# Kernel tuning notes

Hardware: AMD Instinct MI355X
Metric: run time of the kernel (lower is better)

## Reference

```python
import jax, jax.numpy as jnp
import numpy as np
from functools import partial

SEQ, BS, IN, H, A = 1024, 512, 128, 256, 3
NEG_INF = jnp.float32(-1e8)


def setup_inputs() -> dict:
    key = jax.random.key(0)
    ks = jax.random.split(key, 16)
    g = lambda k, shape, s=0.1: (jax.random.normal(k, shape, dtype=jnp.float32) * s)
    inp = {
        "x": jax.random.normal(ks[0], (SEQ * BS, IN), dtype=jnp.float32),
        "done": jax.random.randint(ks[1], (SEQ * BS,), 0, 2, dtype=jnp.int32),
        "invalid_action_mask": jax.random.randint(ks[2], (SEQ * BS, A), 0, 2).astype(bool),
        "h0": jnp.zeros((1, BS, H), jnp.float32),
        "c0": jnp.zeros((1, BS, H), jnp.float32),
        # LSTM params (torch gate order: i, f, g, o)
        "W_ih": g(ks[3], (4 * H, IN)),
        "W_hh": g(ks[4], (4 * H, H)),
        "b_ih": jnp.zeros((4 * H,), jnp.float32),
        "b_hh": jnp.zeros((4 * H,), jnp.float32),
        # action head MLP: H -> H/2 -> H/2 -> A with tanh
        "Wa1": g(ks[5], (H // 2, H)), "ba1": jnp.zeros((H // 2,), jnp.float32),
        "Wa2": g(ks[6], (H // 2, H // 2)), "ba2": jnp.zeros((H // 2,), jnp.float32),
        "Wa3": g(ks[7], (A, H // 2)), "ba3": jnp.zeros((A,), jnp.float32),
        # value head MLP: H -> H/2 -> H/2 -> 1 with tanh
        "Wv1": g(ks[8], (H // 2, H)), "bv1": jnp.zeros((H // 2,), jnp.float32),
        "Wv2": g(ks[9], (H // 2, H // 2)), "bv2": jnp.zeros((H // 2,), jnp.float32),
        "Wv3": g(ks[10], (1, H // 2)), "bv3": jnp.zeros((1,), jnp.float32),
    }
    return inp


def _mlp(h, W1, b1, W2, b2, W3, b3):
    h = jnp.tanh(h @ W1.T + b1)
    h = jnp.tanh(h @ W2.T + b2)
    return h @ W3.T + b3


def _scan_lstm(x, done_f, h0, c0, W_ih, W_hh, b_ih, b_hh):
    batch = h0.shape[1]
    xs = x.reshape(-1, batch, x.shape[-1])        # (T, BS, IN) time-major
    ds = done_f.reshape(-1, batch)                # (T, BS)
    b = b_ih + b_hh

    def step(carry, inp):
        h, c = carry
        xt, dt = inp
        m = (1.0 - dt)[:, None]                   # reset mask before step
        h = h * m
        c = c * m
        gates = xt @ W_ih.T + h @ W_hh.T + b      # (BS, 4H)
        i, f, gg, o = jnp.split(gates, 4, axis=-1)
        c = jax.nn.sigmoid(f) * c + jax.nn.sigmoid(i) * jnp.tanh(gg)
        h = jax.nn.sigmoid(o) * jnp.tanh(c)
        return (h, c), h

    (hn, cn), hs = jax.lax.scan(step, (h0[0], c0[0]), (xs, ds))
    hidden = hs.reshape(-1, h0.shape[-1])         # (T*BS, H), time-major like torch cat
    return hidden, hn[None], cn[None]


def reference(x, done, invalid_action_mask, h0, c0, W_ih, W_hh, b_ih, b_hh,
              Wa1, ba1, Wa2, ba2, Wa3, ba3, Wv1, bv1, Wv2, bv2, Wv3, bv3):
    done_f = done.astype(x.dtype)
    hidden, hn, cn = _scan_lstm(x, done_f, h0, c0, W_ih, W_hh, b_ih, b_hh)
    logits = _mlp(hidden, Wa1, ba1, Wa2, ba2, Wa3, ba3)
    # CategoricalMasked: masks = ~invalid_action_mask, masked logits -> -1e8
    logits = jnp.where(~invalid_action_mask, logits, NEG_INF)
    value = _mlp(hidden, Wv1, bv1, Wv2, bv2, Wv3, bv3)
    return logits, value, hn, cn
```

## Files before the change

### kernel.cpp

```cpp
#include <hip/hip_runtime.h>
#include <hip/hip_bf16.h>
#include <stdint.h>
#include <stddef.h>


typedef short bf16x8 __attribute__((ext_vector_type(8)));
typedef short bf16x4 __attribute__((ext_vector_type(4)));
typedef float f32x4  __attribute__((ext_vector_type(4)));

#define LOG2E 1.44269504088896340736f

__device__ __forceinline__ float fexp2(float x){ return __builtin_amdgcn_exp2f(x); }
__device__ __forceinline__ float frcpf_(float x){ return __builtin_amdgcn_rcpf(x); }
__device__ __forceinline__ float fsig(float x){ return frcpf_(1.0f + fexp2(-x*LOG2E)); }
__device__ __forceinline__ float ftanh_(float x){ return 1.0f - 2.0f*frcpf_(1.0f + fexp2(x*(2.0f*LOG2E))); }

__device__ __forceinline__ short f2bf(float f){
  unsigned u = __builtin_bit_cast(unsigned, f);
  u += 0x7fffu + ((u>>16)&1u);
  return (short)(u>>16);
}
__device__ __forceinline__ float bf2f(short h){
  unsigned u = ((unsigned)(unsigned short)h)<<16;
  return __builtin_bit_cast(float, u);
}

static constexpr size_t WS_WMAIN  = 0;
static constexpr size_t WS_WA1P   = 786432;
static constexpr size_t WS_WV1P   = 851968;
static constexpr size_t WS_WA2P   = 917504;
static constexpr size_t WS_WV2P   = 950272;
static constexpr size_t WS_BMAIN  = 983040;
static constexpr size_t WS_META   = 1048576;
static constexpr size_t WS_SEGS   = 1081344;
static constexpr size_t WS_SORTED = 3178496;
static constexpr size_t WS_HID    = 5275648;
static constexpr size_t WS_NEED_SPLIT = WS_HID + 268435456;

__global__ void k0a_packmain(const float* __restrict__ wih, const float* __restrict__ whh,
                             const float* __restrict__ bih, const float* __restrict__ bhh,
                             short* __restrict__ wp, float* __restrict__ bp)
{
  int tidg = blockIdx.x*512 + threadIdx.x;
  {
    int lane = tidg & 63;
    int nt   = (tidg>>6) & 15;
    int ci   = tidg>>10;
    int kt = ci>>2, gq = ci&3;
    int gs = lane & 15;
    int ug = gs>>2, eg = gs&3;
    int j  = gq*64 + ug*16 + nt;
    int g  = eg*256 + j;
    int k0 = kt*32 + (lane>>4)*8;
    bf16x8 ov;
#pragma unroll
    for (int jj=0;jj<8;++jj){
      int k = k0 + jj;
      float v = (k < 128) ? wih[(size_t)g*128 + k] : whh[(size_t)g*256 + (k-128)];
      ov[jj] = f2bf(v);
    }
    *(bf16x8*)(wp + (size_t)tidg*8) = ov;
  }
  if (tidg < 1024) {
    int cgp = tidg;
    int gq = cgp>>8, nt = (cgp>>4)&15, ug = (cgp>>2)&3, eg = cgp&3;
    int g = eg*256 + gq*64 + ug*16 + nt;
    bp[cgp] = bih[g] + bhh[g];
  }
}

__global__ void k0b_packheads(const float* __restrict__ wa1, const float* __restrict__ wv1,
                              const float* __restrict__ wa2, const float* __restrict__ wv2,
                              short* __restrict__ wa1p, short* __restrict__ wv1p,
                              short* __restrict__ wa2p, short* __restrict__ wv2p)
{
  int p = blockIdx.x*512 + threadIdx.x;
  const float* src; short* dst; int K; int pl;
  if (p < 4096)       { src=wa1; dst=wa1p; K=256; pl=p; }
  else if (p < 8192)  { src=wv1; dst=wv1p; K=256; pl=p-4096; }
  else if (p < 10240) { src=wa2; dst=wa2p; K=128; pl=p-8192; }
  else                { src=wv2; dst=wv2p; K=128; pl=p-10240; }
  int lane = pl & 63;
  int f    = pl >> 6;
  int nt   = f & 7;
  int kt   = f >> 3;
  int n  = nt*16 + (lane&15);
  int k0 = kt*32 + (lane>>4)*8;
  bf16x8 ov;
#pragma unroll
  for (int j=0;j<8;++j) ov[j] = f2bf(src[(size_t)n*K + k0 + j]);
  *(bf16x8*)(dst + (size_t)pl*8) = ov;
}

__global__ void k1_maskmode(const unsigned char* __restrict__ mask, uint32_t* __restrict__ flag)
{
  int i = blockIdx.x*256 + threadIdx.x;
  uint32_t v = ((i & 3) != 0) ? (uint32_t)mask[i] : 0u;
  if (v) atomicOr((unsigned int*)flag, 1u);
}

__global__ void k2a_segments(const int* __restrict__ done, uint32_t* __restrict__ segs,
                             uint32_t* __restrict__ nSegs)
{
  const int b = blockIdx.x;
  const int tid = threadIdx.x;
  __shared__ uint16_t starts[1025];
  __shared__ uint32_t cnts[256];
  __shared__ uint32_t basePos;

  uint32_t my[4]; int myn = 0;
  int t0 = tid*4;
#pragma unroll
  for (int i=0;i<4;++i){
    int t = t0 + i;
    int d = done[(size_t)t*512 + b];
    if (t == 0 || d != 0) my[myn++] = (uint32_t)t;
  }
  cnts[tid] = (uint32_t)myn;
  __syncthreads();
  for (int off=1; off<256; off<<=1){
    uint32_t v = (tid >= off) ? cnts[tid-off] : 0u;
    __syncthreads();
    cnts[tid] += v;
    __syncthreads();
  }
  uint32_t myBase = cnts[tid] - (uint32_t)myn;
  uint32_t ns = cnts[255];
  for (int i=0;i<myn;++i) starts[myBase+i] = (uint16_t)my[i];
  if (tid == 0) {
    starts[ns] = 1024;
    basePos = atomicAdd((unsigned int*)nSegs, ns);
  }
  __syncthreads();
  for (uint32_t i = tid; i < ns; i += 256) {
    uint32_t st = starts[i];
    uint32_t ln = (uint32_t)starts[i+1] - st;
    segs[basePos + i] = ((ln-1u)<<19) | (st<<9) | (uint32_t)b;
  }
}

__global__ void k2b_hist(const uint32_t* __restrict__ segs, const uint32_t* __restrict__ nSegs,
                         uint32_t* __restrict__ hist)
{
  __shared__ uint32_t lh[1025];
  const uint32_t n = *nSegs;
  for (int i = threadIdx.x; i < 1025; i += 512) lh[i] = 0;
  __syncthreads();
  for (uint32_t i = blockIdx.x*512u + threadIdx.x; i < n; i += gridDim.x*512u) {
    uint32_t ln = ((segs[i]>>19)&1023u) + 1u;
    atomicAdd(&lh[ln], 1u);
  }
  __syncthreads();
  for (int i = threadIdx.x; i < 1025; i += 512)
    if (lh[i]) atomicAdd((unsigned int*)&hist[i], lh[i]);
}

__global__ void k2c_scan(const uint32_t* __restrict__ hist, uint32_t* __restrict__ curs)
{
  __shared__ uint32_t s[1024];
  const int tid = threadIdx.x;
  uint32_t own = hist[tid+1];
  s[tid] = own;
  __syncthreads();
  for (int off=1; off<1024; off<<=1){
    uint32_t v = (tid+off < 1024) ? s[tid+off] : 0u;
    __syncthreads();
    s[tid] += v;
    __syncthreads();
  }
  curs[tid+1] = s[tid] - own;
  if (tid == 0) curs[0] = 0;
}

__global__ void k2d_scatter(const uint32_t* __restrict__ segs, const uint32_t* __restrict__ nSegs,
                            uint32_t* __restrict__ curs, uint32_t* __restrict__ sorted)
{
  __shared__ uint32_t lh[1025];
  __shared__ uint32_t base[1025];
  const uint32_t n = *nSegs;
  const uint32_t chunk = (n + 127u) >> 7;
  const uint32_t lo = blockIdx.x * chunk;
  const uint32_t hi = (lo + chunk < n) ? (lo + chunk) : n;
  for (int i = threadIdx.x; i < 1025; i += 512) lh[i] = 0;
  __syncthreads();
  for (uint32_t i = lo + threadIdx.x; i < hi; i += 512u) {
    uint32_t ln = ((segs[i]>>19)&1023u) + 1u;
    atomicAdd(&lh[ln], 1u);
  }
  __syncthreads();
  for (int i = threadIdx.x; i < 1025; i += 512) {
    uint32_t c = lh[i];
    if (c) base[i] = atomicAdd((unsigned int*)&curs[i], c);
    lh[i] = 0;
  }
  __syncthreads();
  for (uint32_t i = lo + threadIdx.x; i < hi; i += 512u) {
    uint32_t r = segs[i];
    uint32_t ln = ((r>>19)&1023u) + 1u;
    uint32_t pos = base[ln] + atomicAdd(&lh[ln], 1u);
    sorted[pos] = r;
  }
}

__global__ __launch_bounds__(512, 2) void k3r_lstm(
    const float* __restrict__ x, const int* __restrict__ done,
    const float* __restrict__ h0, const float* __restrict__ c0,
    const short* __restrict__ wpack, const float* __restrict__ bpack,
    const uint32_t* __restrict__ sortedSegs, const uint32_t* __restrict__ nSegsPtr,
    short* __restrict__ hidden, float* __restrict__ hnOut, float* __restrict__ cnOut)
{
  __shared__ char smem[54016];
  char* Alds = smem;
  float* biasL = (float*)(smem + 49152);
  uint32_t* meta = (uint32_t*)(smem + 53248);

  const int tid  = threadIdx.x;
  const int lane = tid & 63;
  const int wv   = tid >> 6;
  const int gq   = wv & 3;
  const int rh   = wv >> 2;
  const int cl   = lane & 15;
  const int u    = lane >> 4;
  const int ku   = u*16;
  const int swc  = (cl & 7) << 4;
  const int rA   = rh*32 + cl;
  const int rB   = rA + 16;
  const int jb   = gq*64 + u*16;
  const int jb2  = 2*jb;

  const int row8 = tid >> 3;
  const int oct  = tid & 7;
  const int rsw8 = (row8 & 7) << 4;

  biasL[tid]       = bpack[tid];
  biasL[512 + tid] = bpack[512 + tid];

  const uint32_t nSegs = *nSegsPtr;
  const uint32_t nGroups = (nSegs + 63u) >> 6;

  for (uint32_t g = blockIdx.x; g < nGroups; g += gridDim.x) {
    __syncthreads();
    if (tid < 64) {
      uint32_t idx = g*64u + (uint32_t)tid;
      uint32_t b=0, st=0, ln=0;
      if (idx < nSegs) {
        uint32_t r = sortedSegs[idx];
        b = r & 511u; st = (r>>9)&1023u; ln = ((r>>19)&1023u) + 1u;
      }
      meta[tid] = b; meta[64+tid] = st; meta[128+tid] = ln;
    }
    __syncthreads();

    const uint32_t mb8  = meta[row8];
    const uint32_t mst8 = meta[64+row8];
    const uint32_t mln8 = meta[128+row8];
    const uint32_t mbA  = meta[rA],    mbB  = meta[rB];
    const uint32_t mstA = meta[64+rA], mstB = meta[64+rB];
    const uint32_t mlnA = meta[128+rA],mlnB = meta[128+rB];
    const int maxLen = (int)meta[128];

    {
      const bool act = (mln8 > 0u);
      float xf[16];
      if (act) {
        const float4* xp = (const float4*)(x + ((size_t)mst8*512u + mb8)*128u + (size_t)oct*16u);
#pragma unroll
        for (int i=0;i<4;++i){ float4 t4 = xp[i]; xf[4*i]=t4.x; xf[4*i+1]=t4.y; xf[4*i+2]=t4.z; xf[4*i+3]=t4.w; }
      } else {
#pragma unroll
        for (int i=0;i<16;++i) xf[i]=0.0f;
      }
      bf16x8 v0, v1;
#pragma unroll
      for (int j=0;j<8;++j){ v0[j]=f2bf(xf[j]); v1[j]=f2bf(xf[8+j]); }
      *(bf16x8*)(Alds + row8*768 + ((oct*32     ) ^ rsw8)) = v0;
      *(bf16x8*)(Alds + row8*768 + ((oct*32 + 16) ^ rsw8)) = v1;

      const bool useInit = act && (mst8 == 0u) && (done[mb8] == 0);
      float hf[32];
      if (useInit) {
        const float4* hp = (const float4*)(h0 + (size_t)mb8*256u + (size_t)oct*32u);
#pragma unroll
        for (int i=0;i<8;++i){ float4 t4 = hp[i]; hf[4*i]=t4.x; hf[4*i+1]=t4.y; hf[4*i+2]=t4.z; hf[4*i+3]=t4.w; }
      } else {
#pragma unroll
        for (int i=0;i<32;++i) hf[i]=0.0f;
      }
#pragma unroll
      for (int q=0;q<4;++q){
        bf16x8 hv;
#pragma unroll
        for (int j=0;j<8;++j) hv[j]=f2bf(hf[q*8+j]);
        *(bf16x8*)(Alds + row8*768 + ((256 + oct*64 + q*16) ^ rsw8)) = hv;
      }
    }

    float cregA[16], cregB[16];
    {
      const bool initA = (mlnA > 0u) && (mstA == 0u) && (done[mbA] == 0);
      const bool initB = (mlnB > 0u) && (mstB == 0u) && (done[mbB] == 0);
      f32x4 ca[4], cb[4];
#pragma unroll
      for (int q=0;q<4;++q){
        ca[q] = initA ? *(const f32x4*)(c0 + (size_t)mbA*256u + jb + q*4) : (f32x4){0.f,0.f,0.f,0.f};
        cb[q] = initB ? *(const f32x4*)(c0 + (size_t)mbB*256u + jb + q*4) : (f32x4){0.f,0.f,0.f,0.f};
      }
#pragma unroll
      for (int nt=0;nt<16;++nt){ cregA[nt]=ca[nt>>2][nt&3]; cregB[nt]=cb[nt>>2][nt&3]; }
    }

    for (int it = 0; it < maxLen; ++it) {
      __syncthreads();

      if (it >= 1 && (uint32_t)(it-1) < mln8) {
        const size_t grow = (size_t)(mst8 + (uint32_t)(it-1))*512u + mb8;
        short* hp = hidden + grow*256u + (size_t)oct*32u;
#pragma unroll
        for (int q=0;q<4;++q)
          *(bf16x8*)(hp + q*8) = *(const bf16x8*)(Alds + row8*768 + ((256 + oct*64 + q*16) ^ rsw8));
      }

      f32x4 accA[16], accB[16];
#pragma unroll
      for (int nt=0;nt<16;++nt){
        f32x4 bv = *(const f32x4*)(biasL + gq*256 + nt*16 + u*4);
        accA[nt]=bv; accB[nt]=bv;
      }
      for (int kt=0; kt<12; ++kt) {
        if ((kt & 3) == 0) __builtin_amdgcn_s_barrier();
        const short* wkt = wpack + (size_t)(kt*4 + gq)*8192 + lane*8;
        bf16x8 bfA = *(const bf16x8*)(Alds + rA*768 + ((kt*64 + ku) ^ swc));
        bf16x8 bfB = *(const bf16x8*)(Alds + rB*768 + ((kt*64 + ku) ^ swc));
#pragma unroll
        for (int nt=0;nt<16;++nt) {
          const bf16x8 wf = *(const bf16x8*)(wkt + nt*512);
          accA[nt] = __builtin_amdgcn_mfma_f32_16x16x32_bf16(wf, bfA, accA[nt], 0,0,0);
          accB[nt] = __builtin_amdgcn_mfma_f32_16x16x32_bf16(wf, bfB, accB[nt], 0,0,0);
        }
      }

      bf16x8 xpre0, xpre1;
      {
        const bool xact = (it + 1) < (int)mln8;
        if (xact) {
          const float4* xp = (const float4*)(x + ((size_t)(mst8+it+1u)*512u + mb8)*128u + (size_t)oct*16u);
          float4 a0=xp[0], a1=xp[1], a2=xp[2], a3=xp[3];
          xpre0[0]=f2bf(a0.x); xpre0[1]=f2bf(a0.y); xpre0[2]=f2bf(a0.z); xpre0[3]=f2bf(a0.w);
          xpre0[4]=f2bf(a1.x); xpre0[5]=f2bf(a1.y); xpre0[6]=f2bf(a1.z); xpre0[7]=f2bf(a1.w);
          xpre1[0]=f2bf(a2.x); xpre1[1]=f2bf(a2.y); xpre1[2]=f2bf(a2.z); xpre1[3]=f2bf(a2.w);
          xpre1[4]=f2bf(a3.x); xpre1[5]=f2bf(a3.y); xpre1[6]=f2bf(a3.z); xpre1[7]=f2bf(a3.w);
        } else {
#pragma unroll
          for (int j=0;j<8;++j){ xpre0[j]=0; xpre1[j]=0; }
        }
      }

      __syncthreads();

      const bool finA = (it == (int)mlnA - 1) && (mstA + mlnA == 1024u) && (mlnA > 0u);
      const bool finB = (it == (int)mlnB - 1) && (mstB + mlnB == 1024u) && (mlnB > 0u);
      bf16x8 hvA0, hvA1, hvB0, hvB1;
#pragma unroll
      for (int nt=0;nt<16;++nt) {
        f32x4 gA = accA[nt];
        float i0=fsig(gA[0]), f0=fsig(gA[1]), g0=ftanh_(gA[2]), o0=fsig(gA[3]);
        float cA = f0*cregA[nt] + i0*g0; cregA[nt]=cA;
        float hA = o0*ftanh_(cA);
        if (nt < 8) hvA0[nt] = f2bf(hA); else hvA1[nt-8] = f2bf(hA);
        if (finA) { hnOut[(size_t)mbA*256u + jb + nt] = hA; cnOut[(size_t)mbA*256u + jb + nt] = cA; }
        f32x4 gB = accB[nt];
        float i1=fsig(gB[0]), f1=fsig(gB[1]), g1=ftanh_(gB[2]), o1=fsig(gB[3]);
        float cB = f1*cregB[nt] + i1*g1; cregB[nt]=cB;
        float hB = o1*ftanh_(cB);
        if (nt < 8) hvB0[nt] = f2bf(hB); else hvB1[nt-8] = f2bf(hB);
        if (finB) { hnOut[(size_t)mbB*256u + jb + nt] = hB; cnOut[(size_t)mbB*256u + jb + nt] = cB; }
      }
      *(bf16x8*)(Alds + rA*768 + ((256 + jb2     ) ^ swc)) = hvA0;
      *(bf16x8*)(Alds + rA*768 + ((256 + jb2 + 16) ^ swc)) = hvA1;
      *(bf16x8*)(Alds + rB*768 + ((256 + jb2     ) ^ swc)) = hvB0;
      *(bf16x8*)(Alds + rB*768 + ((256 + jb2 + 16) ^ swc)) = hvB1;

      *(bf16x8*)(Alds + row8*768 + ((oct*32     ) ^ rsw8)) = xpre0;
      *(bf16x8*)(Alds + row8*768 + ((oct*32 + 16) ^ rsw8)) = xpre1;
    }

    __syncthreads();
    if (maxLen > 0 && mln8 == (uint32_t)maxLen) {
      const size_t grow = (size_t)(mst8 + (uint32_t)(maxLen-1))*512u + mb8;
      short* hp = hidden + grow*256u + (size_t)oct*32u;
#pragma unroll
      for (int q=0;q<4;++q)
        *(bf16x8*)(hp + q*8) = *(const bf16x8*)(Alds + row8*768 + ((256 + oct*64 + q*16) ^ rsw8));
    }
  }
}

__global__ __launch_bounds__(512, 1) void k4_heads(
    const short* __restrict__ hidden,
    const short* __restrict__ wa1p, const short* __restrict__ wv1p,
    const short* __restrict__ wa2p, const short* __restrict__ wv2p,
    const float* __restrict__ ba1, const float* __restrict__ bv1,
    const float* __restrict__ ba2, const float* __restrict__ bv2,
    const float* __restrict__ wa3, const float* __restrict__ ba3,
    const float* __restrict__ wv3, const float* __restrict__ bv3,
    const unsigned char* __restrict__ maskB, const uint32_t* __restrict__ maskModePtr,
    float* __restrict__ logits, float* __restrict__ value)
{
  __shared__ char smem[67600];
  char* hidL = smem;
  char* hb1  = smem + 32768;
  char* hb2  = smem + 49152;
  float* w3L = (float*)(smem + 65536);
  float* b3L = (float*)(smem + 67584);

  const int tid  = threadIdx.x;
  const int lane = tid & 63;
  const int wv   = tid >> 6;
  const int gq   = wv & 3;
  const int rh   = wv >> 2;
  const int cl   = lane & 15;
  const int u    = lane >> 4;
  const int ku   = u*16;
  const int swc  = (cl & 7) << 4;
  const int row8 = tid >> 3;
  const int oct  = tid & 7;
  const int rsw8 = (row8 & 7) << 4;
  const size_t r0 = (size_t)blockIdx.x * 64u;

  {
    const short* hp = hidden + (r0 + (size_t)row8)*256u + (size_t)oct*32u;
#pragma unroll
    for (int q=0;q<4;++q)
      *(bf16x8*)(hidL + row8*512 + ((oct*64 + q*16) ^ rsw8)) = *(const bf16x8*)(hp + q*8);
  }
  if (tid < 128) {
    w3L[tid]       = wa3[tid];
    w3L[128 + tid] = wa3[128 + tid];
    w3L[256 + tid] = wa3[256 + tid];
    w3L[384 + tid] = wv3[tid];
  }
  if (tid == 0) { b3L[0]=ba3[0]; b3L[1]=ba3[1]; b3L[2]=ba3[2]; b3L[3]=bv3[0]; }
  const uint32_t maskByteMode = *maskModePtr;
  const int* maskI = (const int*)maskB;
  __syncthreads();

  for (int hd = 0; hd < 2; ++hd) {
    const short* w1p = hd ? wv1p : wa1p;
    const short* w2p = hd ? wv2p : wa2p;
    const float* b1  = hd ? bv1 : ba1;
    const float* b2  = hd ? bv2 : ba2;

    {
      f32x4 h1[2][2];
#pragma unroll
      for (int n1=0;n1<2;++n1){
        f32x4 bv = *(const f32x4*)(b1 + gq*32 + n1*16 + u*4);
        h1[n1][0]=bv; h1[n1][1]=bv;
      }
      for (int kt2=0; kt2<8; ++kt2) {
        bf16x8 bh[2];
#pragma unroll
        for (int r4=0;r4<2;++r4)
          bh[r4] = *(const bf16x8*)(hidL + (rh*32 + r4*16 + cl)*512 + ((kt2*64 + ku) ^ swc));
#pragma unroll
        for (int n1=0;n1<2;++n1) {
          const bf16x8 wf = *(const bf16x8*)(w1p + (size_t)(kt2*8 + gq*2 + n1)*512 + lane*8);
#pragma unroll
          for (int r4=0;r4<2;++r4)
            h1[n1][r4] = __builtin_amdgcn_mfma_f32_16x16x32_bf16(wf, bh[r4], h1[n1][r4], 0,0,0);
        }
      }
#pragma unroll
      for (int n1=0;n1<2;++n1){
#pragma unroll
        for (int r4=0;r4<2;++r4){
          bf16x4 hv;
#pragma unroll
          for (int e=0;e<4;++e) hv[e] = f2bf(ftanh_(h1[n1][r4][e]));
          int row = rh*32 + r4*16 + cl;
          *(bf16x4*)(hb1 + row*256 + ((2*(gq*32 + n1*16 + u*4)) ^ swc)) = hv;
        }
      }
    }
    __syncthreads();

    {
      f32x4 h2[2][2];
#pragma unroll
      for (int n1=0;n1<2;++n1){
        f32x4 bv = *(const f32x4*)(b2 + gq*32 + n1*16 + u*4);
        h2[n1][0]=bv; h2[n1][1]=bv;
      }
      for (int kt2=0; kt2<4; ++kt2) {
        bf16x8 bh[2];
#pragma unroll
        for (int r4=0;r4<2;++r4)
          bh[r4] = *(const bf16x8*)(hb1 + (rh*32 + r4*16 + cl)*256 + ((kt2*64 + ku) ^ swc));
#pragma unroll
        for (int n1=0;n1<2;++n1) {
          const bf16x8 wf = *(const bf16x8*)(w2p + (size_t)(kt2*8 + gq*2 + n1)*512 + lane*8);
#pragma unroll
          for (int r4=0;r4<2;++r4)
            h2[n1][r4] = __builtin_amdgcn_mfma_f32_16x16x32_bf16(wf, bh[r4], h2[n1][r4], 0,0,0);
        }
      }
#pragma unroll
      for (int n1=0;n1<2;++n1){
#pragma unroll
        for (int r4=0;r4<2;++r4){
          bf16x4 hv;
#pragma unroll
          for (int e=0;e<4;++e) hv[e] = f2bf(ftanh_(h2[n1][r4][e]));
          int row = rh*32 + r4*16 + cl;
          *(bf16x4*)(hb2 + row*256 + ((2*(gq*32 + n1*16 + u*4)) ^ swc)) = hv;
        }
      }
    }
    __syncthreads();

    {
      const int row  = tid >> 3;
      const int o    = (tid >> 1) & 3;
      const int half = tid & 1;
      const int sw   = (row&7)<<4;
      float s = half ? 0.0f : b3L[o];
      const float* wr = w3L + o*128 + half*64;
#pragma unroll
      for (int k16=0; k16<8; ++k16) {
        bf16x8 av = *(const bf16x8*)(hb2 + row*256 + (((half*8 + k16)*16) ^ sw));
#pragma unroll
        for (int j=0;j<8;++j) s += bf2f(av[j]) * wr[k16*8+j];
      }
      s += __shfl_xor(s, 1);
      if (half == 0) {
        const size_t grow = r0 + (size_t)row;
        if (hd == 0 && o < 3) {
          const size_t mi = grow*3u + (size_t)o;
          const bool masked = maskByteMode ? (maskB[mi] != 0) : (maskI[mi] != 0);
          logits[mi] = masked ? -1e8f : s;
        } else if (hd == 1 && o == 3) {
          value[grow] = s;
        }
      }
    }
    __syncthreads();
  }
}

__global__ __launch_bounds__(512, 2) void k3_lstm_fused(
    const float* __restrict__ x, const int* __restrict__ done,
    const float* __restrict__ h0, const float* __restrict__ c0,
    const short* __restrict__ wpack, const float* __restrict__ bpack,
    const short* __restrict__ wa1p, const short* __restrict__ wv1p,
    const short* __restrict__ wa2p, const short* __restrict__ wv2p,
    const float* __restrict__ ba1, const float* __restrict__ bv1,
    const float* __restrict__ ba2, const float* __restrict__ bv2,
    const float* __restrict__ wa3, const float* __restrict__ ba3,
    const float* __restrict__ wv3, const float* __restrict__ bv3,
    const unsigned char* __restrict__ maskB,
    const uint32_t* __restrict__ maskModePtr,
    const uint32_t* __restrict__ sortedSegs, const uint32_t* __restrict__ nSegsPtr,
    float* __restrict__ logits, float* __restrict__ value,
    float* __restrict__ hnOut, float* __restrict__ cnOut)
{
  __shared__ char smem[121616];
  char* Alds = smem;
  char* hb1  = smem + 49152;
  char* hb2  = smem + 81920;
  float* biasL = (float*)(smem + 114688);
  uint32_t* meta = (uint32_t*)(smem + 118784);
  float* w3L = (float*)(smem + 119552);
  float* b3L = (float*)(smem + 121600);

  const int tid  = threadIdx.x;
  const int lane = tid & 63;
  const int wv   = tid >> 6;
  const int gq   = wv & 3;
  const int hd   = wv >> 2;
  const int cl   = lane & 15;
  const int u    = lane >> 4;
  const int ku   = u*16;
  const int swc  = (cl & 7) << 4;
  const int rA   = hd*32 + cl;
  const int rB   = rA + 16;
  const int jb   = gq*64 + u*16;
  const int jb2  = 2*jb;

  const int row8 = tid >> 3;
  const int oct  = tid & 7;
  const int rsw8 = (row8 & 7) << 4;

  biasL[tid]       = bpack[tid];
  biasL[512 + tid] = bpack[512 + tid];
  if (tid < 128) {
    w3L[tid]       = wa3[tid];
    w3L[128 + tid] = wa3[128 + tid];
    w3L[256 + tid] = wa3[256 + tid];
    w3L[384 + tid] = wv3[tid];
  }
  if (tid == 0) { b3L[0]=ba3[0]; b3L[1]=ba3[1]; b3L[2]=ba3[2]; b3L[3]=bv3[0]; }

  float4 bH1v[2], bH2v[2];
  {
    const float* b1 = hd ? bv1 : ba1;
    const float* b2 = hd ? bv2 : ba2;
#pragma unroll
    for (int n1=0; n1<2; ++n1) {
      bH1v[n1] = *(const float4*)(b1 + gq*32 + n1*16 + u*4);
      bH2v[n1] = *(const float4*)(b2 + gq*32 + n1*16 + u*4);
    }
  }
  const short* w1p = hd ? wv1p : wa1p;
  const short* w2p = hd ? wv2p : wa2p;

  const uint32_t maskByteMode = *maskModePtr;
  const int* maskI = (const int*)maskB;

  const uint32_t nSegs = *nSegsPtr;
  const uint32_t nGroups = (nSegs + 63u) >> 6;

  for (uint32_t g = blockIdx.x; g < nGroups; g += gridDim.x) {
    __syncthreads();
    if (tid < 64) {
      uint32_t idx = g*64u + (uint32_t)tid;
      uint32_t b=0, st=0, ln=0;
      if (idx < nSegs) {
        uint32_t r = sortedSegs[idx];
        b = r & 511u; st = (r>>9)&1023u; ln = ((r>>19)&1023u) + 1u;
      }
      meta[tid] = b; meta[64+tid] = st; meta[128+tid] = ln;
    }
    __syncthreads();

    const uint32_t mb8  = meta[row8];
    const uint32_t mst8 = meta[64+row8];
    const uint32_t mln8 = meta[128+row8];
    const uint32_t mbA  = meta[rA],    mbB  = meta[rB];
    const uint32_t mstA = meta[64+rA], mstB = meta[64+rB];
    const uint32_t mlnA = meta[128+rA],mlnB = meta[128+rB];
    const int maxLen = (int)meta[128];

    {
      const bool act = (mln8 > 0u);
      float xf[16];
      if (act) {
        const float4* xp = (const float4*)(x + ((size_t)mst8*512u + mb8)*128u + (size_t)oct*16u);
#pragma unroll
        for (int i=0;i<4;++i){ float4 t4 = xp[i]; xf[4*i]=t4.x; xf[4*i+1]=t4.y; xf[4*i+2]=t4.z; xf[4*i+3]=t4.w; }
      } else {
#pragma unroll
        for (int i=0;i<16;++i) xf[i]=0.0f;
      }
      bf16x8 v0, v1;
#pragma unroll
      for (int j=0;j<8;++j){ v0[j]=f2bf(xf[j]); v1[j]=f2bf(xf[8+j]); }
      *(bf16x8*)(Alds + row8*768 + ((oct*32     ) ^ rsw8)) = v0;
      *(bf16x8*)(Alds + row8*768 + ((oct*32 + 16) ^ rsw8)) = v1;

      const bool useInit = act && (mst8 == 0u) && (done[mb8] == 0);
      float hf[32];
      if (useInit) {
        const float4* hp = (const float4*)(h0 + (size_t)mb8*256u + (size_t)oct*32u);
#pragma unroll
        for (int i=0;i<8;++i){ float4 t4 = hp[i]; hf[4*i]=t4.x; hf[4*i+1]=t4.y; hf[4*i+2]=t4.z; hf[4*i+3]=t4.w; }
      } else {
#pragma unroll
        for (int i=0;i<32;++i) hf[i]=0.0f;
      }
#pragma unroll
      for (int q=0;q<4;++q){
        bf16x8 hv;
#pragma unroll
        for (int j=0;j<8;++j) hv[j]=f2bf(hf[q*8+j]);
        *(bf16x8*)(Alds + row8*768 + ((256 + oct*64 + q*16) ^ rsw8)) = hv;
      }
    }

    float cregA[16], cregB[16];
    {
      const bool initA = (mlnA > 0u) && (mstA == 0u) && (done[mbA] == 0);
      const bool initB = (mlnB > 0u) && (mstB == 0u) && (done[mbB] == 0);
      f32x4 ca[4], cb[4];
#pragma unroll
      for (int q=0;q<4;++q){
        ca[q] = initA ? *(const f32x4*)(c0 + (size_t)mbA*256u + jb + q*4) : (f32x4){0.f,0.f,0.f,0.f};
        cb[q] = initB ? *(const f32x4*)(c0 + (size_t)mbB*256u + jb + q*4) : (f32x4){0.f,0.f,0.f,0.f};
      }
#pragma unroll
      for (int nt=0;nt<16;++nt){ cregA[nt]=ca[nt>>2][nt&3]; cregB[nt]=cb[nt>>2][nt&3]; }
    }

    for (int it = 0; it < maxLen; ++it) {
      __syncthreads();

      f32x4 accA[16], accB[16];
#pragma unroll
      for (int nt=0;nt<16;++nt){
        f32x4 bv = *(const f32x4*)(biasL + gq*256 + nt*16 + u*4);
        accA[nt]=bv; accB[nt]=bv;
      }
      for (int kt=0; kt<12; ++kt) {
        if ((kt & 3) == 0) __builtin_amdgcn_s_barrier();
        const short* wkt = wpack + (size_t)(kt*4 + gq)*8192 + lane*8;
        bf16x8 bfA = *(const bf16x8*)(Alds + rA*768 + ((kt*64 + ku) ^ swc));
        bf16x8 bfB = *(const bf16x8*)(Alds + rB*768 + ((kt*64 + ku) ^ swc));
#pragma unroll
        for (int nt=0;nt<16;++nt) {
          const bf16x8 wf = *(const bf16x8*)(wkt + nt*512);
          accA[nt] = __builtin_amdgcn_mfma_f32_16x16x32_bf16(wf, bfA, accA[nt], 0,0,0);
          accB[nt] = __builtin_amdgcn_mfma_f32_16x16x32_bf16(wf, bfB, accB[nt], 0,0,0);
        }
      }

      float4 xq0,xq1,xq2,xq3;
      {
        const bool xact = (it + 1) < (int)mln8;
        if (xact) {
          const float4* xp = (const float4*)(x + ((size_t)(mst8+it+1u)*512u + mb8)*128u + (size_t)oct*16u);
          xq0=xp[0]; xq1=xp[1]; xq2=xp[2]; xq3=xp[3];
        } else {
          xq0=xq1=xq2=xq3=make_float4(0.f,0.f,0.f,0.f);
        }
      }

      __syncthreads();

      float hfA[16], hfB[16];
#pragma unroll
      for (int nt=0;nt<16;++nt) {
        f32x4 gA = accA[nt];
        float i0=fsig(gA[0]), f0=fsig(gA[1]), g0=ftanh_(gA[2]), o0=fsig(gA[3]);
        float cA = f0*cregA[nt] + i0*g0; cregA[nt]=cA; hfA[nt] = o0*ftanh_(cA);
        f32x4 gB = accB[nt];
        float i1=fsig(gB[0]), f1=fsig(gB[1]), g1=ftanh_(gB[2]), o1=fsig(gB[3]);
        float cB = f1*cregB[nt] + i1*g1; cregB[nt]=cB; hfB[nt] = o1*ftanh_(cB);
      }
      {
        bf16x8 hv0, hv1;
#pragma unroll
        for (int q=0;q<8;++q){ hv0[q]=f2bf(hfA[q]); hv1[q]=f2bf(hfA[8+q]); }
        *(bf16x8*)(Alds + rA*768 + ((256 + jb2     ) ^ swc)) = hv0;
        *(bf16x8*)(Alds + rA*768 + ((256 + jb2 + 16) ^ swc)) = hv1;
#pragma unroll
        for (int q=0;q<8;++q){ hv0[q]=f2bf(hfB[q]); hv1[q]=f2bf(hfB[8+q]); }
        *(bf16x8*)(Alds + rB*768 + ((256 + jb2     ) ^ swc)) = hv0;
        *(bf16x8*)(Alds + rB*768 + ((256 + jb2 + 16) ^ swc)) = hv1;
      }
      if ((it == (int)mlnA - 1) && (mstA + mlnA == 1024u)) {
        float4* hp4 = (float4*)(hnOut + (size_t)mbA*256u + jb);
        float4* cp4 = (float4*)(cnOut + (size_t)mbA*256u + jb);
#pragma unroll
        for (int q=0;q<4;++q){
          hp4[q] = make_float4(hfA[4*q],hfA[4*q+1],hfA[4*q+2],hfA[4*q+3]);
          cp4[q] = make_float4(cregA[4*q],cregA[4*q+1],cregA[4*q+2],cregA[4*q+3]);
        }
      }
      if ((it == (int)mlnB - 1) && (mstB + mlnB == 1024u)) {
        float4* hp4 = (float4*)(hnOut + (size_t)mbB*256u + jb);
        float4* cp4 = (float4*)(cnOut + (size_t)mbB*256u + jb);
#pragma unroll
        for (int q=0;q<4;++q){
          hp4[q] = make_float4(hfB[4*q],hfB[4*q+1],hfB[4*q+2],hfB[4*q+3]);
          cp4[q] = make_float4(cregB[4*q],cregB[4*q+1],cregB[4*q+2],cregB[4*q+3]);
        }
      }
      {
        float xf[16];
        xf[0]=xq0.x; xf[1]=xq0.y; xf[2]=xq0.z; xf[3]=xq0.w;
        xf[4]=xq1.x; xf[5]=xq1.y; xf[6]=xq1.z; xf[7]=xq1.w;
        xf[8]=xq2.x; xf[9]=xq2.y; xf[10]=xq2.z; xf[11]=xq2.w;
        xf[12]=xq3.x; xf[13]=xq3.y; xf[14]=xq3.z; xf[15]=xq3.w;
        bf16x8 v0, v1;
#pragma unroll
        for (int j=0;j<8;++j){ v0[j]=f2bf(xf[j]); v1[j]=f2bf(xf[8+j]); }
        *(bf16x8*)(Alds + row8*768 + ((oct*32     ) ^ rsw8)) = v0;
        *(bf16x8*)(Alds + row8*768 + ((oct*32 + 16) ^ rsw8)) = v1;
      }

      __syncthreads();

      {
        f32x4 h1[2][4];
#pragma unroll
        for (int n1=0;n1<2;++n1){
          f32x4 bv = {bH1v[n1].x, bH1v[n1].y, bH1v[n1].z, bH1v[n1].w};
#pragma unroll
          for (int r4=0;r4<4;++r4) h1[n1][r4] = bv;
        }
        for (int kt2=0; kt2<8; ++kt2) {
          bf16x8 bh[4];
#pragma unroll
          for (int r4=0;r4<4;++r4)
            bh[r4] = *(const bf16x8*)(Alds + (r4*16+cl)*768 + ((256 + kt2*64 + ku) ^ swc));
#pragma unroll
          for (int n1=0;n1<2;++n1) {
            const bf16x8 wf = *(const bf16x8*)(w1p + (size_t)(kt2*8 + gq*2 + n1)*512 + lane*8);
#pragma unroll
            for (int r4=0;r4<4;++r4)
              h1[n1][r4] = __builtin_amdgcn_mfma_f32_16x16x32_bf16(wf, bh[r4], h1[n1][r4], 0,0,0);
          }
        }
#pragma unroll
        for (int n1=0;n1<2;++n1){
#pragma unroll
          for (int r4=0;r4<4;++r4){
            bf16x4 hv;
#pragma unroll
            for (int e=0;e<4;++e) hv[e] = f2bf(ftanh_(h1[n1][r4][e]));
            int row = r4*16 + cl;
            *(bf16x4*)(hb1 + hd*16384 + row*256 + ((2*(gq*32 + n1*16 + u*4)) ^ swc)) = hv;
          }
        }
      }
      __syncthreads();

      {
        f32x4 h2[2][4];
#pragma unroll
        for (int n1=0;n1<2;++n1){
          f32x4 bv = {bH2v[n1].x, bH2v[n1].y, bH2v[n1].z, bH2v[n1].w};
#pragma unroll
          for (int r4=0;r4<4;++r4) h2[n1][r4] = bv;
        }
        const char* hbIn = hb1 + hd*16384;
        for (int kt2=0; kt2<4; ++kt2) {
          bf16x8 bh[4];
#pragma unroll
          for (int r4=0;r4<4;++r4)
            bh[r4] = *(const bf16x8*)(hbIn + (r4*16+cl)*256 + ((kt2*64 + ku) ^ swc));
#pragma unroll
          for (int n1=0;n1<2;++n1) {
            const bf16x8 wf = *(const bf16x8*)(w2p + (size_t)(kt2*8 + gq*2 + n1)*512 + lane*8);
#pragma unroll
            for (int r4=0;r4<4;++r4)
              h2[n1][r4] = __builtin_amdgcn_mfma_f32_16x16x32_bf16(wf, bh[r4], h2[n1][r4], 0,0,0);
          }
        }
#pragma unroll
        for (int n1=0;n1<2;++n1){
#pragma unroll
          for (int r4=0;r4<4;++r4){
            bf16x4 hv;
#pragma unroll
            for (int e=0;e<4;++e) hv[e] = f2bf(ftanh_(h2[n1][r4][e]));
            int row = r4*16 + cl;
            *(bf16x4*)(hb2 + hd*16384 + row*256 + ((2*(gq*32 + n1*16 + u*4)) ^ swc)) = hv;
          }
        }
      }
      __syncthreads();

      {
        const int frow = tid >> 3;
        const int o    = (tid >> 1) & 3;
        const int half = tid & 1;
        const uint32_t fmb  = meta[frow];
        const uint32_t fmst = meta[64+frow];
        const uint32_t fmln = meta[128+frow];
        const char* srcb = (o < 3) ? hb2 : (hb2 + 16384);
        const int sw = (frow&7)<<4;
        float s = half ? 0.0f : b3L[o];
        const float* wr = w3L + o*128 + half*64;
#pragma unroll
        for (int k16=0; k16<8; ++k16) {
          bf16x8 av = *(const bf16x8*)(srcb + frow*256 + (((half*8 + k16)*16) ^ sw));
#pragma unroll
          for (int j=0;j<8;++j) s += bf2f(av[j]) * wr[k16*8+j];
        }
        s += __shfl_xor(s, 1);
        if (half == 0 && it < (int)fmln) {
          const size_t grow = (size_t)((int)fmst + it)*512u + fmb;
          if (o < 3) {
            const size_t mi = grow*3u + (size_t)o;
            const bool masked = maskByteMode ? (maskB[mi] != 0) : (maskI[mi] != 0);
            logits[mi] = masked ? -1e8f : s;
          } else {
            value[grow] = s;
          }
        }
      }
    }
  }
}

extern "C" void kernel_launch(void* const* d_in, const int* in_sizes, int n_in,
                              void* d_out, int out_size, void* d_ws, size_t ws_size,
                              hipStream_t stream) {
  const float* x    = (const float*)d_in[0];
  const int*   done = (const int*)d_in[1];
  const unsigned char* mask = (const unsigned char*)d_in[2];
  const float* h0   = (const float*)d_in[3];
  const float* c0   = (const float*)d_in[4];
  const float* wih  = (const float*)d_in[5];
  const float* whh  = (const float*)d_in[6];
  const float* bih  = (const float*)d_in[7];
  const float* bhh  = (const float*)d_in[8];
  const float* wa1  = (const float*)d_in[9];
  const float* ba1  = (const float*)d_in[10];
  const float* wa2  = (const float*)d_in[11];
  const float* ba2  = (const float*)d_in[12];
  const float* wa3  = (const float*)d_in[13];
  const float* ba3  = (const float*)d_in[14];
  const float* wv1  = (const float*)d_in[15];
  const float* bv1  = (const float*)d_in[16];
  const float* wv2  = (const float*)d_in[17];
  const float* bv2  = (const float*)d_in[18];
  const float* wv3  = (const float*)d_in[19];
  const float* bv3  = (const float*)d_in[20];

  char* ws = (char*)d_ws;
  float* outLogits = (float*)d_out;
  float* outValue  = outLogits + 1572864;
  float* outHn     = outValue  + 524288;
  float* outCn     = outHn     + 131072;

  hipMemsetAsync(ws + WS_META, 0, 16384, stream);

  k0a_packmain<<<96, 512, 0, stream>>>(wih, whh, bih, bhh,
      (short*)(ws + WS_WMAIN), (float*)(ws + WS_BMAIN));
  k0b_packheads<<<24, 512, 0, stream>>>(wa1, wv1, wa2, wv2,
      (short*)(ws + WS_WA1P), (short*)(ws + WS_WV1P),
      (short*)(ws + WS_WA2P), (short*)(ws + WS_WV2P));

  k1_maskmode<<<64, 256, 0, stream>>>(mask, (uint32_t*)(ws + WS_META + 16));

  k2a_segments<<<512, 256, 0, stream>>>(done, (uint32_t*)(ws + WS_SEGS),
                                        (uint32_t*)(ws + WS_META));
  k2b_hist<<<128, 512, 0, stream>>>((const uint32_t*)(ws + WS_SEGS),
      (const uint32_t*)(ws + WS_META), (uint32_t*)(ws + WS_META + 4096));
  k2c_scan<<<1, 1024, 0, stream>>>((const uint32_t*)(ws + WS_META + 4096),
      (uint32_t*)(ws + WS_META + 12288));
  k2d_scatter<<<128, 512, 0, stream>>>((const uint32_t*)(ws + WS_SEGS),
      (const uint32_t*)(ws + WS_META), (uint32_t*)(ws + WS_META + 12288),
      (uint32_t*)(ws + WS_SORTED));

  if (ws_size >= WS_NEED_SPLIT) {
    k3r_lstm<<<256, 512, 0, stream>>>(x, done, h0, c0,
        (const short*)(ws + WS_WMAIN), (const float*)(ws + WS_BMAIN),
        (const uint32_t*)(ws + WS_SORTED), (const uint32_t*)(ws + WS_META),
        (short*)(ws + WS_HID), outHn, outCn);
    k4_heads<<<8192, 512, 0, stream>>>((const short*)(ws + WS_HID),
        (const short*)(ws + WS_WA1P), (const short*)(ws + WS_WV1P),
        (const short*)(ws + WS_WA2P), (const short*)(ws + WS_WV2P),
        ba1, bv1, ba2, bv2, wa3, ba3, wv3, bv3,
        mask, (const uint32_t*)(ws + WS_META + 16),
        outLogits, outValue);
  } else {
    k3_lstm_fused<<<256, 512, 0, stream>>>(x, done, h0, c0,
        (const short*)(ws + WS_WMAIN), (const float*)(ws + WS_BMAIN),
        (const short*)(ws + WS_WA1P), (const short*)(ws + WS_WV1P),
        (const short*)(ws + WS_WA2P), (const short*)(ws + WS_WV2P),
        ba1, bv1, ba2, bv2, wa3, ba3, wv3, bv3,
        mask, (const uint32_t*)(ws + WS_META + 16),
        (const uint32_t*)(ws + WS_SORTED), (const uint32_t*)(ws + WS_META),
        outLogits, outValue, outHn, outCn);
  }

  (void)in_sizes; (void)n_in; (void)out_size;
}
```

Measured before the change: 1.397 ms.

## Stream LSTM weights through LDS with async global-to-LDS double buffering

The recurrent LSTM kernel now moves packed weights into a double-buffered LDS staging area with global_load_lds, using explicit vmcnt waits, instead of loading them from global memory straight into registers. Each wave now owns a 32-column gate slice across all 64 rows, and a new weight packing layout matches that slice. The next timestep's x rows are prefetched asynchronously into LDS. Bias is added after the MFMAs, and s_setprio is raised around the MFMA blocks. This targets global weight-load latency on the serial recurrence critical path. In exchange, LDS use grows to about 149KB, which drops occupancy to one block per CU despite launch_bounds(512,2), and correctness now rests on hand-written waitcnt counts.

```diff
diff --git a/kernel.cpp b/kernel.cpp
--- a/kernel.cpp
+++ b/kernel.cpp
@@ -23,6 +23,12 @@
 __device__ __forceinline__ float bf2f(short h){
   unsigned u = ((unsigned)(unsigned short)h)<<16;
   return __builtin_bit_cast(float, u);
+}
+
+__device__ __forceinline__ void gload16(const void* g, void* l) {
+  __builtin_amdgcn_global_load_lds(
+      (const __attribute__((address_space(1))) unsigned int*)g,
+      (__attribute__((address_space(3))) unsigned int*)l, 16, 0, 0);
 }
 
 static constexpr size_t WS_WMAIN  = 0;
@@ -40,6 +46,39 @@
 __global__ void k0a_packmain(const float* __restrict__ wih, const float* __restrict__ whh,
                              const float* __restrict__ bih, const float* __restrict__ bhh,
                              short* __restrict__ wp, float* __restrict__ bp)
+{
+  int tidg = blockIdx.x*512 + threadIdx.x;
+  {
+    int lane = tidg & 63;
+    int ntl  = (tidg>>6) & 3;
+    int gq   = (tidg>>8) & 7;
+    int hc   = tidg >> 11;
+    int kt = hc >> 1, nh = hc & 1;
+    int nt = nh*4 + ntl;
+    int slot = lane & 15;
+    int ug = slot >> 2, eg = slot & 3;
+    int j  = gq*32 + ug*8 + nt;
+    int g  = eg*256 + j;
+    int k0 = kt*32 + (lane>>4)*8;
+    bf16x8 ov;
+#pragma unroll
+    for (int jj=0;jj<8;++jj){
+      int k = k0 + jj;
+      float v = (k < 128) ? wih[(size_t)g*128 + k] : whh[(size_t)g*256 + (k-128)];
+      ov[jj] = f2bf(v);
+    }
+    *(bf16x8*)(wp + (size_t)tidg*8) = ov;
+  }
+  if (tidg < 1024) {
+    int j = tidg>>2, e = tidg&3;
+    int g = e*256 + j;
+    bp[tidg] = bih[g] + bhh[g];
+  }
+}
+
+__global__ void k0a_packmain_v4(const float* __restrict__ wih, const float* __restrict__ whh,
+                                const float* __restrict__ bih, const float* __restrict__ bhh,
+                                short* __restrict__ wp, float* __restrict__ bp)
 {
   int tidg = blockIdx.x*512 + threadIdx.x;
   {
@@ -209,24 +248,21 @@
     const uint32_t* __restrict__ sortedSegs, const uint32_t* __restrict__ nSegsPtr,
     short* __restrict__ hidden, float* __restrict__ hnOut, float* __restrict__ cnOut)
 {
-  __shared__ char smem[54016];
-  char* Alds = smem;
-  float* biasL = (float*)(smem + 49152);
-  uint32_t* meta = (uint32_t*)(smem + 53248);
+  __shared__ char smem[152320];
+  char*  Alds  = smem;
+  char*  wbuf  = smem + 49152;
+  char*  xbuf  = smem + 114688;
+  float* biasL = (float*)(smem + 147456);
+  uint32_t* meta = (uint32_t*)(smem + 151552);
 
   const int tid  = threadIdx.x;
   const int lane = tid & 63;
   const int wv   = tid >> 6;
-  const int gq   = wv & 3;
-  const int rh   = wv >> 2;
   const int cl   = lane & 15;
   const int u    = lane >> 4;
   const int ku   = u*16;
   const int swc  = (cl & 7) << 4;
-  const int rA   = rh*32 + cl;
-  const int rB   = rA + 16;
-  const int jb   = gq*64 + u*16;
-  const int jb2  = 2*jb;
+  const int jbL  = wv*32 + u*8;
 
   const int row8 = tid >> 3;
   const int oct  = tid & 7;
@@ -254,9 +290,12 @@
     const uint32_t mb8  = meta[row8];
     const uint32_t mst8 = meta[64+row8];
     const uint32_t mln8 = meta[128+row8];
-    const uint32_t mbA  = meta[rA],    mbB  = meta[rB];
-    const uint32_t mstA = meta[64+rA], mstB = meta[64+rB];
-    const uint32_t mlnA = meta[128+rA],mlnB = meta[128+rB];
+    uint32_t mbR[4], mstR[4], mlnR[4];
+#pragma unroll
+    for (int r4=0;r4<4;++r4){
+      int r = r4*16 + cl;
+      mbR[r4] = meta[r]; mstR[r4] = meta[64+r]; mlnR[r4] = meta[128+r];
+    }
     const int maxLen = (int)meta[128];
 
     {
@@ -295,18 +334,14 @@
       }
     }
 
-    float cregA[16], cregB[16];
-    {
-      const bool initA = (mlnA > 0u) && (mstA == 0u) && (done[mbA] == 0);
-      const bool initB = (mlnB > 0u) && (mstB == 0u) && (done[mbB] == 0);
-      f32x4 ca[4], cb[4];
-#pragma unroll
-      for (int q=0;q<4;++q){
-        ca[q] = initA ? *(const f32x4*)(c0 + (size_t)mbA*256u + jb + q*4) : (f32x4){0.f,0.f,0.f,0.f};
-        cb[q] = initB ? *(const f32x4*)(c0 + (size_t)mbB*256u + jb + q*4) : (f32x4){0.f,0.f,0.f,0.f};
-      }
-#pragma unroll
-      for (int nt=0;nt<16;++nt){ cregA[nt]=ca[nt>>2][nt&3]; cregB[nt]=cb[nt>>2][nt&3]; }
+    float creg[4][8];
+#pragma unroll
+    for (int r4=0;r4<4;++r4){
+      const bool initR = (mlnR[r4] > 0u) && (mstR[r4] == 0u) && (done[mbR[r4]] == 0);
+      f32x4 c01 = initR ? *(const f32x4*)(c0 + (size_t)mbR[r4]*256u + jbL    ) : (f32x4){0.f,0.f,0.f,0.f};
+      f32x4 c23 = initR ? *(const f32x4*)(c0 + (size_t)mbR[r4]*256u + jbL + 4) : (f32x4){0.f,0.f,0.f,0.f};
+#pragma unroll
+      for (int q=0;q<4;++q){ creg[r4][q] = c01[q]; creg[r4][4+q] = c23[q]; }
     }
 
     for (int it = 0; it < maxLen; ++it) {
@@ -319,66 +354,104 @@
         for (int q=0;q<4;++q)
           *(bf16x8*)(hp + q*8) = *(const bf16x8*)(Alds + row8*768 + ((256 + oct*64 + q*16) ^ rsw8));
       }
-
-      f32x4 accA[16], accB[16];
-#pragma unroll
-      for (int nt=0;nt<16;++nt){
-        f32x4 bv = *(const f32x4*)(biasL + gq*256 + nt*16 + u*4);
-        accA[nt]=bv; accB[nt]=bv;
-      }
-      for (int kt=0; kt<12; ++kt) {
-        if ((kt & 3) == 0) __builtin_amdgcn_s_barrier();
-        const short* wkt = wpack + (size_t)(kt*4 + gq)*8192 + lane*8;
-        bf16x8 bfA = *(const bf16x8*)(Alds + rA*768 + ((kt*64 + ku) ^ swc));
-        bf16x8 bfB = *(const bf16x8*)(Alds + rB*768 + ((kt*64 + ku) ^ swc));
-#pragma unroll
-        for (int nt=0;nt<16;++nt) {
-          const bf16x8 wf = *(const bf16x8*)(wkt + nt*512);
-          accA[nt] = __builtin_amdgcn_mfma_f32_16x16x32_bf16(wf, bfA, accA[nt], 0,0,0);
-          accB[nt] = __builtin_amdgcn_mfma_f32_16x16x32_bf16(wf, bfB, accB[nt], 0,0,0);
-        }
-      }
+      asm volatile("" ::: "memory");
+
+      const char* wsrc = (const char*)wpack;
+      {
+        const char* s0 = wsrc + 0*32768 + wv*4096;
+        const char* s1 = wsrc + 1*32768 + wv*4096;
+        char* d0 = wbuf + 0*32768 + wv*4096;
+        char* d1 = wbuf + 1*32768 + wv*4096;
+#pragma unroll
+        for (int q=0;q<4;++q) gload16(s0 + q*1024 + lane*16, d0 + q*1024);
+#pragma unroll
+        for (int q=0;q<4;++q) gload16(s1 + q*1024 + lane*16, d1 + q*1024);
+      }
+      {
+        uint32_t trow = mst8 + (uint32_t)it + 1u;
+        if (trow > 1023u) trow = 0u;
+        const float* xsrc = x + ((size_t)trow*512u + mb8)*128u + (size_t)oct*16u;
+#pragma unroll
+        for (int q=0;q<4;++q) gload16(xsrc + q*4, xbuf + wv*4096 + q*1024);
+      }
+
+      f32x4 acc[4][8];
+      bf16x8 bfA[4];
+#pragma unroll
+      for (int s = 0; s < 24; ++s) {
+        const int kt = s >> 1;
+        const int nh = s & 1;
+        if (s < 2)        asm volatile("s_waitcnt vmcnt(8)" ::: "memory");
+        else if (s == 23) asm volatile("s_waitcnt vmcnt(0)" ::: "memory");
+        else              asm volatile("s_waitcnt vmcnt(4)" ::: "memory");
+        __builtin_amdgcn_sched_barrier(0);
+        if (nh == 0) {
+#pragma unroll
+          for (int r4=0;r4<4;++r4)
+            bfA[r4] = *(const bf16x8*)(Alds + (r4*16+cl)*768 + ((kt*64 + ku) ^ swc));
+        }
+        const char* wb = wbuf + (s&1)*32768 + wv*4096;
+        bf16x8 wf[4];
+#pragma unroll
+        for (int q=0;q<4;++q) wf[q] = *(const bf16x8*)(wb + q*1024 + lane*16);
+        __builtin_amdgcn_s_setprio(1);
+#pragma unroll
+        for (int q=0;q<4;++q) {
+          const int nt = nh*4 + q;
+#pragma unroll
+          for (int r4=0;r4<4;++r4) {
+            if (kt == 0) {
+              f32x4 z = {0.f,0.f,0.f,0.f};
+              acc[r4][nt] = __builtin_amdgcn_mfma_f32_16x16x32_bf16(wf[q], bfA[r4], z, 0,0,0);
+            } else {
+              acc[r4][nt] = __builtin_amdgcn_mfma_f32_16x16x32_bf16(wf[q], bfA[r4], acc[r4][nt], 0,0,0);
+            }
+          }
+        }
+        __builtin_amdgcn_s_setprio(0);
+        __builtin_amdgcn_sched_barrier(0);
+        if (s < 22) {
+          const int hc = s + 2;
+          const char* sw_ = wsrc + (size_t)hc*32768 + wv*4096;
+          char* dw_ = wbuf + (s&1)*32768 + wv*4096;
+#pragma unroll
+          for (int q=0;q<4;++q) gload16(sw_ + q*1024 + lane*16, dw_ + q*1024);
+        }
+      }
+
+      __syncthreads();
 
       bf16x8 xpre0, xpre1;
       {
-        const bool xact = (it + 1) < (int)mln8;
-        if (xact) {
-          const float4* xp = (const float4*)(x + ((size_t)(mst8+it+1u)*512u + mb8)*128u + (size_t)oct*16u);
-          float4 a0=xp[0], a1=xp[1], a2=xp[2], a3=xp[3];
-          xpre0[0]=f2bf(a0.x); xpre0[1]=f2bf(a0.y); xpre0[2]=f2bf(a0.z); xpre0[3]=f2bf(a0.w);
-          xpre0[4]=f2bf(a1.x); xpre0[5]=f2bf(a1.y); xpre0[6]=f2bf(a1.z); xpre0[7]=f2bf(a1.w);
-          xpre1[0]=f2bf(a2.x); xpre1[1]=f2bf(a2.y); xpre1[2]=f2bf(a2.z); xpre1[3]=f2bf(a2.w);
-          xpre1[4]=f2bf(a3.x); xpre1[5]=f2bf(a3.y); xpre1[6]=f2bf(a3.z); xpre1[7]=f2bf(a3.w);
-        } else {
-#pragma unroll
-          for (int j=0;j<8;++j){ xpre0[j]=0; xpre1[j]=0; }
-        }
-      }
-
-      __syncthreads();
-
-      const bool finA = (it == (int)mlnA - 1) && (mstA + mlnA == 1024u) && (mlnA > 0u);
-      const bool finB = (it == (int)mlnB - 1) && (mstB + mlnB == 1024u) && (mlnB > 0u);
-      bf16x8 hvA0, hvA1, hvB0, hvB1;
-#pragma unroll
-      for (int nt=0;nt<16;++nt) {
-        f32x4 gA = accA[nt];
-        float i0=fsig(gA[0]), f0=fsig(gA[1]), g0=ftanh_(gA[2]), o0=fsig(gA[3]);
-        float cA = f0*cregA[nt] + i0*g0; cregA[nt]=cA;
-        float hA = o0*ftanh_(cA);
-        if (nt < 8) hvA0[nt] = f2bf(hA); else hvA1[nt-8] = f2bf(hA);
-        if (finA) { hnOut[(size_t)mbA*256u + jb + nt] = hA; cnOut[(size_t)mbA*256u + jb + nt] = cA; }
-        f32x4 gB = accB[nt];
-        float i1=fsig(gB[0]), f1=fsig(gB[1]), g1=ftanh_(gB[2]), o1=fsig(gB[3]);
-        float cB = f1*cregB[nt] + i1*g1; cregB[nt]=cB;
-        float hB = o1*ftanh_(cB);
-        if (nt < 8) hvB0[nt] = f2bf(hB); else hvB1[nt-8] = f2bf(hB);
-        if (finB) { hnOut[(size_t)mbB*256u + jb + nt] = hB; cnOut[(size_t)mbB*256u + jb + nt] = cB; }
-      }
-      *(bf16x8*)(Alds + rA*768 + ((256 + jb2     ) ^ swc)) = hvA0;
-      *(bf16x8*)(Alds + rA*768 + ((256 + jb2 + 16) ^ swc)) = hvA1;
-      *(bf16x8*)(Alds + rB*768 + ((256 + jb2     ) ^ swc)) = hvB0;
-      *(bf16x8*)(Alds + rB*768 + ((256 + jb2 + 16) ^ swc)) = hvB1;
+        f32x4 xq0 = *(const f32x4*)(xbuf + wv*4096 + 0*1024 + lane*16);
+        f32x4 xq1 = *(const f32x4*)(xbuf + wv*4096 + 1*1024 + lane*16);
+        f32x4 xq2 = *(const f32x4*)(xbuf + wv*4096 + 2*1024 + lane*16);
+        f32x4 xq3 = *(const f32x4*)(xbuf + wv*4096 + 3*1024 + lane*16);
+#pragma unroll
+        for (int q=0;q<4;++q){ xpre0[q]=f2bf(xq0[q]); xpre0[4+q]=f2bf(xq1[q]); }
+#pragma unroll
+        for (int q=0;q<4;++q){ xpre1[q]=f2bf(xq2[q]); xpre1[4+q]=f2bf(xq3[q]); }
+      }
+
+#pragma unroll
+      for (int r4=0;r4<4;++r4) {
+        const bool fin = (it == (int)mlnR[r4] - 1) && (mstR[r4] + mlnR[r4] == 1024u) && (mlnR[r4] > 0u);
+        bf16x8 hvv;
+#pragma unroll
+        for (int nt=0;nt<8;++nt) {
+          f32x4 b4 = *(const f32x4*)(biasL + (jbL + nt)*4);
+          f32x4 gA = acc[r4][nt] + b4;
+          float i0=fsig(gA[0]), f0=fsig(gA[1]), g0=ftanh_(gA[2]), o0=fsig(gA[3]);
+          float c = f0*creg[r4][nt] + i0*g0; creg[r4][nt] = c;
+          float h = o0*ftanh_(c);
+          hvv[nt] = f2bf(h);
+          if (fin) {
+            hnOut[(size_t)mbR[r4]*256u + jbL + nt] = h;
+            cnOut[(size_t)mbR[r4]*256u + jbL + nt] = c;
+          }
+        }
+        *(bf16x8*)(Alds + (r4*16+cl)*768 + ((256 + 2*jbL) ^ swc)) = hvv;
+      }
 
       *(bf16x8*)(Alds + row8*768 + ((oct*32     ) ^ rsw8)) = xpre0;
       *(bf16x8*)(Alds + row8*768 + ((oct*32 + 16) ^ rsw8)) = xpre1;
@@ -916,8 +989,6 @@
 
   hipMemsetAsync(ws + WS_META, 0, 16384, stream);
 
-  k0a_packmain<<<96, 512, 0, stream>>>(wih, whh, bih, bhh,
-      (short*)(ws + WS_WMAIN), (float*)(ws + WS_BMAIN));
   k0b_packheads<<<24, 512, 0, stream>>>(wa1, wv1, wa2, wv2,
       (short*)(ws + WS_WA1P), (short*)(ws + WS_WV1P),
       (short*)(ws + WS_WA2P), (short*)(ws + WS_WV2P));
@@ -935,6 +1006,8 @@
       (uint32_t*)(ws + WS_SORTED));
 
   if (ws_size >= WS_NEED_SPLIT) {
+    k0a_packmain<<<96, 512, 0, stream>>>(wih, whh, bih, bhh,
+        (short*)(ws + WS_WMAIN), (float*)(ws + WS_BMAIN));
     k3r_lstm<<<256, 512, 0, stream>>>(x, done, h0, c0,
         (const short*)(ws + WS_WMAIN), (const float*)(ws + WS_BMAIN),
         (const uint32_t*)(ws + WS_SORTED), (const uint32_t*)(ws + WS_META),
@@ -946,6 +1019,8 @@
         mask, (const uint32_t*)(ws + WS_META + 16),
         outLogits, outValue);
   } else {
+    k0a_packmain_v4<<<96, 512, 0, stream>>>(wih, whh, bih, bhh,
+        (short*)(ws + WS_WMAIN), (float*)(ws + WS_BMAIN));
     k3_lstm_fused<<<256, 512, 0, stream>>>(x, done, h0, c0,
         (const short*)(ws + WS_WMAIN), (const float*)(ws + WS_BMAIN),
         (const short*)(ws + WS_WA1P), (const short*)(ws + WS_WV1P),
```

Measured after the change: 2.288 ms. 1.64x slower.
